# Kernel tuning notes

Hardware: AMD Instinct MI355X
Metric: run time of the kernel (lower is better)

The kernel has to match this reference:

```python
import jax, jax.numpy as jnp
import numpy as np

WH, WW, NUM_HEADS = 7, 7, 16
DIM = 512
B_WINDOWS = 4096   # batch * num_windows
NW = 64            # num_windows per image (mask groups)
N = WH * WW        # 49 tokens per window


def _relative_position_index():
    # Mirrors the torch buffer construction exactly (torch.meshgrid default is 'ij').
    coords = np.stack(np.meshgrid(np.arange(WH), np.arange(WW), indexing='ij'))  # [2,WH,WW]
    cf = coords.reshape(2, -1)                              # [2, N]
    rel = cf[:, :, None] - cf[:, None, :]                   # [2, N, N]
    rel = rel.transpose(1, 2, 0).copy()                     # [N, N, 2]
    rel[:, :, 0] += WH - 1
    rel[:, :, 1] += WW - 1
    rel[:, :, 0] *= 2 * WW - 1
    return jnp.asarray(rel.sum(-1), dtype=jnp.int32)        # [N, N]

REL_IDX = _relative_position_index()


def setup_inputs() -> dict:
    key = jax.random.key(0)
    ks = jax.random.split(key, 7)
    return {
        'x':          jax.random.normal(ks[0], (B_WINDOWS, N, DIM), jnp.float32),
        'mask':       jax.random.normal(ks[1], (NW, N, N), jnp.float32),
        'Wqkv':       jax.random.normal(ks[2], (3 * DIM, DIM), jnp.float32) * (DIM ** -0.5),
        'bqkv':       jax.random.normal(ks[3], (3 * DIM,), jnp.float32) * 0.02,
        'bias_table': jax.random.normal(ks[4], ((2 * WH - 1) * (2 * WW - 1), NUM_HEADS), jnp.float32) * 0.02,
        'Wproj':      jax.random.normal(ks[5], (DIM, DIM), jnp.float32) * (DIM ** -0.5),
        'bproj':      jax.random.normal(ks[6], (DIM,), jnp.float32) * 0.02,
    }


def reference(x, mask, Wqkv, bqkv, bias_table, Wproj, bproj):
    B, n, C = x.shape                      # [B_, 49, 512]
    hd = C // NUM_HEADS
    scale = hd ** -0.5
    qkv = (x @ Wqkv.T + bqkv).reshape(B, n, 3, NUM_HEADS, hd)
    qkv = qkv.transpose(2, 0, 3, 1, 4)     # [3, B, H, N, hd]
    q, k, v = qkv[0] * scale, qkv[1], qkv[2]
    attn = jnp.einsum('bhnd,bhmd->bhnm', q, k)          # [B, H, N, N]
    # gathered relative position bias: [1, H, N, N]
    bias = bias_table[REL_IDX].transpose(2, 0, 1)[None]
    attn = attn + bias
    nW = mask.shape[0]
    attn = attn.reshape(B // nW, nW, NUM_HEADS, n, n) + mask[None, :, None]
    attn = jax.nn.softmax(attn.reshape(B, NUM_HEADS, n, n), axis=-1)
    out = jnp.einsum('bhnm,bhmd->bhnd', attn, v)        # [B, H, N, hd]
    out = out.transpose(0, 2, 1, 3).reshape(B, n, C)
    return out @ Wproj.T + bproj
```

## Files before the change

kernel.cpp:

```cpp
#include <hip/hip_runtime.h>
#include <stdint.h>

#define NHEADS 16
#define DIM 512
#define BWIN 4096
#define NTOK 49
#define M_TOTAL (BWIN * NTOK)
#define QSCALE 0.17677669529663687f

typedef __attribute__((ext_vector_type(4)))  float f32x4;
typedef __attribute__((ext_vector_type(16))) float f32x16;
typedef __attribute__((ext_vector_type(8)))  short s16x8;
typedef __attribute__((ext_vector_type(4)))  short s16x4;

__device__ __forceinline__ f32x4 mfma16(s16x8 a, s16x8 b, f32x4 c) {
    return __builtin_amdgcn_mfma_f32_16x16x32_bf16(a, b, c, 0, 0, 0);
}
__device__ __forceinline__ f32x16 mfma32(s16x8 a, s16x8 b, f32x16 c) {
    return __builtin_amdgcn_mfma_f32_32x32x16_bf16(a, b, c, 0, 0, 0);
}

__device__ __forceinline__ short f2bf(float f) {
    unsigned u = __builtin_bit_cast(unsigned, f);
    u += 0x7FFFu + ((u >> 16) & 1u);
    return (short)(u >> 16);
}

__device__ __forceinline__ unsigned cvtpk(float a, float b) {
    unsigned r;
    asm("v_cvt_pk_bf16_f32 %0, %1, %2" : "=v"(r) : "v"(a), "v"(b));
    return r;
}

__device__ __forceinline__ void gload16(const void* g, void* l) {
    __builtin_amdgcn_global_load_lds(
        (const __attribute__((address_space(1))) void*)g,
        (__attribute__((address_space(3))) void*)l, 16, 0, 0);
}


__global__ void k_prep_x(const float* __restrict__ x, short* __restrict__ xb) {
    int i = blockIdx.x * blockDim.x + threadIdx.x;
    int stride = gridDim.x * blockDim.x;
    const int n4 = M_TOTAL * DIM / 4;
    for (; i < n4; i += stride) {
        f32x4 v = ((const f32x4*)x)[i];
        s16x4 o;
        o[0] = f2bf(v[0]); o[1] = f2bf(v[1]); o[2] = f2bf(v[2]); o[3] = f2bf(v[3]);
        ((s16x4*)xb)[i] = o;
    }
}

__global__ void k_prep_w(const float* __restrict__ src, short* __restrict__ dst,
                         int n, int scale_lim) {
    int i = blockIdx.x * blockDim.x + threadIdx.x;
    int stride = gridDim.x * blockDim.x;
    for (; i < n; i += stride) {
        float v = src[i];
        if (i < scale_lim) v *= QSCALE;
        dst[i] = f2bf(v);
    }
}

__global__ void k_prep_bm(const float* __restrict__ btab, const float* __restrict__ mask,
                          float* __restrict__ bmF) {
    int idx = blockIdx.x * blockDim.x + threadIdx.x;
    int stride = gridDim.x * blockDim.x;
    const int n = 64 * NHEADS * 2 * 2 * 64 * 16;
    for (; idx < n; idx += stride) {
        int r    = idx & 15;
        int lane = (idx >> 4) & 63;
        int it   = (idx >> 10) & 1;
        int jt   = (idx >> 11) & 1;
        int head = (idx >> 12) & 15;
        int w64  = idx >> 16;
        int l31 = lane & 31, h = lane >> 5;
        int i = 32 * it + l31;
        int j = 32 * jt + (r & 3) + 8 * (r >> 2) + 4 * h;
        float v;
        if (j >= 49)      v = -1e30f;
        else if (i >= 49) v = 0.f;
        else {
            int ridx = (i / 7 - j / 7 + 6) * 13 + (i % 7 - j % 7 + 6);
            v = btab[ridx * 16 + head] + mask[(w64 * 49 + i) * 49 + j];
        }
        bmF[idx] = v;
    }
}

template <int MODE>
__global__ __launch_bounds__(512, 2) void k_gemm(
    const short* __restrict__ A, const short* __restrict__ B,
    const float* __restrict__ bias, void* __restrict__ C,
    int ntiles, int nwg) {
    __shared__ short lA[2][256 * 64];
    __shared__ short lB[2][256 * 64];
    const int K = 512;
    const size_t MP = M_TOTAL;

    int bid   = blockIdx.x;
    int chunk = nwg >> 3;
    int wg    = (bid & 7) * chunk + (bid >> 3);
    int mt = wg / ntiles;
    int nt = wg - mt * ntiles;

    int t = threadIdx.x;
    int lane = t & 63, wid = t >> 6;
    int l15 = lane & 15, g = (lane >> 4) & 3;
    int wr = wid >> 2, wc = wid & 3;

    const short* aT = A + (size_t)mt * 256 * K;
    const short* bT = B + (size_t)nt * 256 * K;

    f32x4 acc[8][4] = {};
    s16x8 af[4][2], bf0[2][2], bf1[2][2];

#define STAGE_A(buf, H, kt) do {                                               \
    _Pragma("unroll") for (int j = 0; j < 2; j++) {                            \
        int r_ = j * 128 + (H) * 64 + (t >> 3);                                \
        int sc_ = (t & 7) ^ (r_ & 7);                                          \
        gload16(aT + (size_t)r_ * K + (kt) * 64 + sc_ * 8,                     \
                &lA[buf][r_ * 64 + (t & 7) * 8]);                              \
    } } while (0)

#define STAGE_B(buf, H, kt) do {                                               \
    _Pragma("unroll") for (int j = 0; j < 2; j++) {                            \
        int u_ = j * 64 + (t >> 3);                                            \
        int r_ = ((u_ >> 5) << 6) | ((H) << 5) | (u_ & 31);                    \
        int sc_ = (t & 7) ^ (r_ & 7);                                          \
        gload16(bT + (size_t)r_ * K + (kt) * 64 + sc_ * 8,                     \
                &lB[buf][r_ * 64 + (t & 7) * 8]);                              \
    } } while (0)

#define LDA(MH, cur) do {                                                      \
    const short* pa_ = &lA[cur][(wr * 128 + (MH) * 64 + l15) * 64];            \
    _Pragma("unroll") for (int mi = 0; mi < 4; mi++)                           \
    _Pragma("unroll") for (int ks = 0; ks < 2; ks++)                           \
        af[mi][ks] = *(const s16x8*)(pa_ + mi * 1024 +                         \
                                     (((ks * 4 + g) ^ (l15 & 7)) * 8));        \
    } while (0)

#define LDB(BF, NH, cur) do {                                                  \
    const short* pb_ = &lB[cur][(wc * 64 + (NH) * 32 + l15) * 64];             \
    _Pragma("unroll") for (int nj = 0; nj < 2; nj++)                           \
    _Pragma("unroll") for (int ks = 0; ks < 2; ks++)                           \
        BF[nj][ks] = *(const s16x8*)(pb_ + nj * 1024 +                         \
                                     (((ks * 4 + g) ^ (l15 & 7)) * 8));        \
    } while (0)

#define MMQ(BF, MH, NH) do {                                                   \
    __builtin_amdgcn_s_setprio(1);                                             \
    _Pragma("unroll") for (int ks = 0; ks < 2; ks++)                           \
    _Pragma("unroll") for (int mi = 0; mi < 4; mi++)                           \
    _Pragma("unroll") for (int nj = 0; nj < 2; nj++)                           \
        acc[(MH) * 4 + mi][(NH) * 2 + nj] =                                    \
            mfma16(af[mi][ks], BF[nj][ks], acc[(MH) * 4 + mi][(NH) * 2 + nj]); \
    __builtin_amdgcn_s_setprio(0);                                             \
} while (0)

#define BAR() __builtin_amdgcn_s_barrier()
#define LGW() do { asm volatile("s_waitcnt lgkmcnt(0)" ::: "memory");          \
                   __builtin_amdgcn_sched_barrier(0); } while (0)
#define VMW(st) do {                                                           \
    if (st) asm volatile("s_waitcnt vmcnt(4)" ::: "memory");                   \
    else    asm volatile("s_waitcnt vmcnt(0)" ::: "memory"); } while (0)

    STAGE_A(0, 0, 0);
    STAGE_B(0, 0, 0);
    STAGE_B(0, 1, 0);
    STAGE_A(0, 1, 0);
    asm volatile("s_waitcnt vmcnt(4)" ::: "memory");
    BAR();

    for (int kt = 0; kt < 8; ++kt) {
        const int cur = kt & 1, nxt = cur ^ 1;
        const bool st = kt < 7;
        LDA(0, cur); LDB(bf0, 0, cur);
        if (st) STAGE_A(nxt, 0, kt + 1);
        VMW(st); BAR(); LGW();
        MMQ(bf0, 0, 0);
        BAR();
        LDB(bf1, 1, cur);
        if (st) STAGE_B(nxt, 0, kt + 1);
        VMW(st); BAR(); LGW();
        MMQ(bf1, 0, 1);
        BAR();
        LDA(1, cur);
        if (st) STAGE_B(nxt, 1, kt + 1);
        VMW(st); BAR(); LGW();
        MMQ(bf1, 1, 1);
        BAR();
        if (st) STAGE_A(nxt, 1, kt + 1);
        VMW(st); BAR(); LGW();
        MMQ(bf0, 1, 0);
        BAR();
    }

#undef STAGE_A
#undef STAGE_B
#undef LDA
#undef LDB
#undef MMQ
#undef BAR
#undef LGW
#undef VMW

    int m0 = mt * 256 + wr * 128;
    int n0 = nt * 256 + wc * 64;

    if (MODE == 0) {
        short* region = (wid < 4) ? (&lA[0][0] + wid * 8192)
                                  : (&lB[0][0] + (wid - 4) * 8192);
#pragma unroll
        for (int a = 0; a < 4; a++) {
            int co = (a >> 1) * 32 + (a & 1) * 16;
            int n = n0 + co + l15;
            float bv = bias[n];
            if (n < 512) bv *= QSCALE;
            int w16 = (co >> 3) + (l15 >> 3);
#pragma unroll
            for (int mi = 0; mi < 8; mi++)
#pragma unroll
                for (int r = 0; r < 4; r++) {
                    int row = mi * 16 + g * 4 + r;
                    region[row * 64 + ((w16 ^ (row & 7)) * 8) + (l15 & 7)] =
                        f2bf(acc[mi][a][r] + bv);
                }
        }
#pragma unroll
        for (int p = 0; p < 2; p++) {
            int plane = (n0 >> 5) + p;
            short* dst = (short*)C + ((size_t)plane * MP + m0) * 32;
#pragma unroll
            for (int i = 0; i < 8; i++) {
                int f = i * 64 + lane;
                int row = f >> 2, c = f & 3;
                s16x8 v = *(const s16x8*)(region + row * 64 +
                                          (((p * 4 + c) ^ (row & 7)) * 8));
                *(s16x8*)(dst + (size_t)f * 8) = v;
            }
        }
    } else {
#pragma unroll
        for (int a = 0; a < 4; a++) {
            int co = (a >> 1) * 32 + (a & 1) * 16;
            int n = n0 + co + l15;
            float bv = bias[n];
#pragma unroll
            for (int mi = 0; mi < 8; mi++)
#pragma unroll
                for (int r = 0; r < 4; r++) {
                    int m = m0 + mi * 16 + g * 4 + r;
                    ((float*)C)[(size_t)m * 512 + n] = acc[mi][a][r] + bv;
                }
        }
    }
}

__global__ __launch_bounds__(256, 4) void k_attn(
    const short* __restrict__ qkv, const float* __restrict__ bmF,
    short* __restrict__ ao) {
    int wid = threadIdx.x >> 6, lane = threadIdx.x & 63;
    int p = blockIdx.x * 4 + wid;
    int w = p >> 4, head = p & 15;
    int l31 = lane & 31, h = lane >> 5;
    const size_t MP = M_TOTAL;

    const short* qb = qkv + ((size_t)head * MP + w * 49) * 32;
    const short* kb = qb + (size_t)16 * MP * 32;
    const short* vb = qb + (size_t)32 * MP * 32;

    s16x8 qf[2][2], kf[2][2];
#pragma unroll
    for (int t = 0; t < 2; t++) {
        int row = t * 32 + l31;
#pragma unroll
        for (int s = 0; s < 2; s++) {
            qf[t][s] = *(const s16x8*)(qb + row * 32 + 16 * s + 8 * h);
            kf[t][s] = *(const s16x8*)(kb + row * 32 + 16 * s + 8 * h);
        }
    }

    union U8 { short s[8]; s16x8 v; };
    U8 vf[4];
#pragma unroll
    for (int jc = 0; jc < 4; jc++)
#pragma unroll
        for (int e = 0; e < 8; e++)
            vf[jc].s[e] = vb[(16 * jc + 8 * h + e) * 32 + l31];

    f32x16 st[2][2] = {};
#pragma unroll
    for (int s = 0; s < 2; s++)
#pragma unroll
        for (int jt = 0; jt < 2; jt++)
#pragma unroll
            for (int it = 0; it < 2; it++)
                st[jt][it] = mfma32(kf[jt][s], qf[it][s], st[jt][it]);

    const float* bs = bmF + ((size_t)((w & 63) * NHEADS + head)) * 4096;
#pragma unroll
    for (int jt = 0; jt < 2; jt++)
#pragma unroll
        for (int it = 0; it < 2; it++) {
            const f32x4* bp = (const f32x4*)(bs + (((jt * 2 + it) * 64) + lane) * 16);
            f32x4 b0 = bp[0], b1 = bp[1], b2 = bp[2], b3 = bp[3];
#pragma unroll
            for (int r = 0; r < 4; r++) {
                st[jt][it][r]      += b0[r];
                st[jt][it][4 + r]  += b1[r];
                st[jt][it][8 + r]  += b2[r];
                st[jt][it][12 + r] += b3[r];
            }
        }

    float inv[2];
#pragma unroll
    for (int it = 0; it < 2; it++) {
        float mx = -1e30f;
#pragma unroll
        for (int jt = 0; jt < 2; jt++)
#pragma unroll
            for (int r = 0; r < 16; r++) mx = fmaxf(mx, st[jt][it][r]);
        mx = fmaxf(mx, __shfl_xor(mx, 32));
        float sum = 0.f;
#pragma unroll
        for (int jt = 0; jt < 2; jt++)
#pragma unroll
            for (int r = 0; r < 16; r++) {
                float e = __expf(st[jt][it][r] - mx);
                st[jt][it][r] = e;
                sum += e;
            }
        sum += __shfl_xor(sum, 32);
        inv[it] = 1.0f / sum;
    }

    f32x16 oacc[2] = {};
#pragma unroll
    for (int jc = 0; jc < 4; jc++) {
        const int jt = jc >> 1, rb = 8 * (jc & 1);
#pragma unroll
        for (int it = 0; it < 2; it++) {
            float iv = inv[it];
            unsigned pk0  = cvtpk(st[jt][it][rb + 0] * iv, st[jt][it][rb + 1] * iv);
            unsigned pk0b = cvtpk(st[jt][it][rb + 2] * iv, st[jt][it][rb + 3] * iv);
            unsigned pk1  = cvtpk(st[jt][it][rb + 4] * iv, st[jt][it][rb + 5] * iv);
            unsigned pk1b = cvtpk(st[jt][it][rb + 6] * iv, st[jt][it][rb + 7] * iv);
            unsigned o0  = __shfl_xor(pk0, 32);
            unsigned o0b = __shfl_xor(pk0b, 32);
            unsigned o1  = __shfl_xor(pk1, 32);
            unsigned o1b = __shfl_xor(pk1b, 32);
            union { unsigned d[4]; s16x8 v; } pa;
            pa.d[0] = h ? o1  : pk0;
            pa.d[1] = h ? o1b : pk0b;
            pa.d[2] = h ? pk1 : o0;
            pa.d[3] = h ? pk1b : o0b;
            oacc[it] = mfma32(pa.v, vf[jc].v, oacc[it]);
        }
    }

    short* ob = ao + (size_t)w * 49 * 512 + head * 32 + l31;
#pragma unroll
    for (int it = 0; it < 2; it++)
#pragma unroll
        for (int r = 0; r < 16; r++) {
            int i = 32 * it + 4 * h + (r & 3) + 8 * (r >> 2);
            if (i < 49) ob[(size_t)i * 512] = f2bf(oacc[it][r]);
        }
}


extern "C" void kernel_launch(void* const* d_in, const int* in_sizes, int n_in,
                              void* d_out, int out_size, void* d_ws, size_t ws_size,
                              hipStream_t stream) {
    const float* x     = (const float*)d_in[0];
    const float* mask  = (const float*)d_in[1];
    const float* Wqkv  = (const float*)d_in[2];
    const float* bqkv  = (const float*)d_in[3];
    const float* btab  = (const float*)d_in[4];
    const float* Wproj = (const float*)d_in[5];
    const float* bproj = (const float*)d_in[6];
    float* out = (float*)d_out;

    char* ws = (char*)d_ws;
    size_t off = 0;
    short* xb     = (short*)(ws + off); off += (size_t)M_TOTAL * 512 * 2;
    short* qkvb   = (short*)(ws + off); off += (size_t)48 * M_TOTAL * 32 * 2 + 65536;
    short* Wqkvb  = (short*)(ws + off); off += (size_t)1536 * 512 * 2;
    short* Wprojb = (short*)(ws + off); off += (size_t)512 * 512 * 2;
    float* bmF    = (float*)(ws + off); off += (size_t)64 * NHEADS * 4 * 64 * 16 * 4;
    short* ao = xb;

    k_prep_x<<<2048, 256, 0, stream>>>(x, xb);
    k_prep_w<<<1536, 256, 0, stream>>>(Wqkv, Wqkvb, 1536 * 512, 512 * 512);
    k_prep_w<<<512, 256, 0, stream>>>(Wproj, Wprojb, 512 * 512, 0);
    k_prep_bm<<<4096, 256, 0, stream>>>(btab, mask, bmF);

    k_gemm<0><<<4704, 512, 0, stream>>>(xb, Wqkvb, bqkv, qkvb, 6, 4704);
    k_attn<<<16384, 256, 0, stream>>>(qkvb, bmF, ao);
    k_gemm<1><<<1568, 512, 0, stream>>>(ao, Wprojb, bproj, out, 2, 1568);
}
```

Baseline: 1.049 ms.

## Fuse fp32-to-bf16 conversion of x into the QKV GEMM A-tile load path

Removes the separate k_prep_x kernel. The QKV GEMM now reads x in fp32 into registers, converts it to bf16 with v_cvt_pk_bf16_f32 and writes it into swizzled LDS, with the global loads rescheduled around the existing double-buffered pipeline. This avoids one full read of x and one write and read of a bf16 copy. In exchange, every N-tile block re-reads and re-converts its A rows in fp32, which doubles A-side bytes unless L2 catches the reuse. A-tile loads now pass through VGPRs instead of going straight to LDS, which raises register pressure under the 2-blocks-per-CU launch bound.

```diff
diff --git a/kernel.cpp b/kernel.cpp
--- a/kernel.cpp
+++ b/kernel.cpp
@@ -38,18 +38,6 @@
         (__attribute__((address_space(3))) void*)l, 16, 0, 0);
 }
 
-
-__global__ void k_prep_x(const float* __restrict__ x, short* __restrict__ xb) {
-    int i = blockIdx.x * blockDim.x + threadIdx.x;
-    int stride = gridDim.x * blockDim.x;
-    const int n4 = M_TOTAL * DIM / 4;
-    for (; i < n4; i += stride) {
-        f32x4 v = ((const f32x4*)x)[i];
-        s16x4 o;
-        o[0] = f2bf(v[0]); o[1] = f2bf(v[1]); o[2] = f2bf(v[2]); o[3] = f2bf(v[3]);
-        ((s16x4*)xb)[i] = o;
-    }
-}
 
 __global__ void k_prep_w(const float* __restrict__ src, short* __restrict__ dst,
                          int n, int scale_lim) {
@@ -90,7 +78,8 @@
 
 template <int MODE>
 __global__ __launch_bounds__(512, 2) void k_gemm(
-    const short* __restrict__ A, const short* __restrict__ B,
+    const float* __restrict__ Af, const short* __restrict__ Ab,
+    const short* __restrict__ B,
     const float* __restrict__ bias, void* __restrict__ C,
     int ntiles, int nwg) {
     __shared__ short lA[2][256 * 64];
@@ -109,17 +98,19 @@
     int l15 = lane & 15, g = (lane >> 4) & 3;
     int wr = wid >> 2, wc = wid & 3;
 
-    const short* aT = A + (size_t)mt * 256 * K;
-    const short* bT = B + (size_t)nt * 256 * K;
+    const float* aTf = Af + (size_t)mt * 256 * K;
+    const short* aTb = Ab + (size_t)mt * 256 * K;
+    const short* bT  = B  + (size_t)nt * 256 * K;
 
     f32x4 acc[8][4] = {};
     s16x8 af[4][2], bf0[2][2], bf1[2][2];
+    f32x4 rh0[2][2], rh1[2][2];
 
 #define STAGE_A(buf, H, kt) do {                                               \
     _Pragma("unroll") for (int j = 0; j < 2; j++) {                            \
         int r_ = j * 128 + (H) * 64 + (t >> 3);                                \
         int sc_ = (t & 7) ^ (r_ & 7);                                          \
-        gload16(aT + (size_t)r_ * K + (kt) * 64 + sc_ * 8,                     \
+        gload16(aTb + (size_t)r_ * K + (kt) * 64 + sc_ * 8,                    \
                 &lA[buf][r_ * 64 + (t & 7) * 8]);                              \
     } } while (0)
 
@@ -130,6 +121,24 @@
         int sc_ = (t & 7) ^ (r_ & 7);                                          \
         gload16(bT + (size_t)r_ * K + (kt) * 64 + sc_ * 8,                     \
                 &lB[buf][r_ * 64 + (t & 7) * 8]);                              \
+    } } while (0)
+
+#define LOADA_F(R, H, kt) do {                                                 \
+    _Pragma("unroll") for (int j = 0; j < 2; j++) {                            \
+        int r_ = j * 128 + (H) * 64 + (t >> 3);                                \
+        const float* p_ = aTf + (size_t)r_ * K + (kt) * 64 + (t & 7) * 8;      \
+        R[j][0] = *(const f32x4*)p_; R[j][1] = *(const f32x4*)(p_ + 4);        \
+    } } while (0)
+
+#define WRA_F(buf, H, R) do {                                                  \
+    _Pragma("unroll") for (int j = 0; j < 2; j++) {                            \
+        int r_ = j * 128 + (H) * 64 + (t >> 3);                                \
+        union { unsigned d[4]; s16x8 v; } u_;                                  \
+        u_.d[0] = cvtpk(R[j][0][0], R[j][0][1]);                               \
+        u_.d[1] = cvtpk(R[j][0][2], R[j][0][3]);                               \
+        u_.d[2] = cvtpk(R[j][1][0], R[j][1][1]);                               \
+        u_.d[3] = cvtpk(R[j][1][2], R[j][1][3]);                               \
+        *(s16x8*)(&lA[buf][r_ * 64 + (((t & 7) ^ (r_ & 7)) * 8)]) = u_.v;      \
     } } while (0)
 
 #define LDA(MH, cur) do {                                                      \
@@ -161,54 +170,95 @@
 #define BAR() __builtin_amdgcn_s_barrier()
 #define LGW() do { asm volatile("s_waitcnt lgkmcnt(0)" ::: "memory");          \
                    __builtin_amdgcn_sched_barrier(0); } while (0)
-#define VMW(st) do {                                                           \
-    if (st) asm volatile("s_waitcnt vmcnt(4)" ::: "memory");                   \
-    else    asm volatile("s_waitcnt vmcnt(0)" ::: "memory"); } while (0)
-
-    STAGE_A(0, 0, 0);
-    STAGE_B(0, 0, 0);
-    STAGE_B(0, 1, 0);
-    STAGE_A(0, 1, 0);
-    asm volatile("s_waitcnt vmcnt(4)" ::: "memory");
-    BAR();
-
-    for (int kt = 0; kt < 8; ++kt) {
-        const int cur = kt & 1, nxt = cur ^ 1;
-        const bool st = kt < 7;
-        LDA(0, cur); LDB(bf0, 0, cur);
-        if (st) STAGE_A(nxt, 0, kt + 1);
-        VMW(st); BAR(); LGW();
-        MMQ(bf0, 0, 0);
+#define VMWN(n) asm volatile("s_waitcnt vmcnt(" #n ")" ::: "memory")
+
+    if constexpr (MODE == 0) {
+        LOADA_F(rh0, 0, 0);
+        LOADA_F(rh1, 1, 0);
+        STAGE_B(0, 0, 0);
+        STAGE_B(0, 1, 0);
+        VMWN(8);  WRA_F(0, 0, rh0);
+        VMWN(4);  WRA_F(0, 1, rh1);
+        VMWN(2);
+        LGW();
         BAR();
-        LDB(bf1, 1, cur);
-        if (st) STAGE_B(nxt, 0, kt + 1);
-        VMW(st); BAR(); LGW();
-        MMQ(bf1, 0, 1);
+
+        for (int kt = 0; kt < 8; ++kt) {
+            const int cur = kt & 1, nxt = cur ^ 1;
+            const bool st = kt < 7;
+            LDA(0, cur); LDB(bf0, 0, cur);
+            if (st) { LOADA_F(rh0, 0, kt + 1); VMWN(4); }
+            else    VMWN(0);
+            BAR(); LGW();
+            MMQ(bf0, 0, 0);
+            BAR();
+            LDB(bf1, 1, cur);
+            if (st) { LOADA_F(rh1, 1, kt + 1); STAGE_B(nxt, 0, kt + 1); VMWN(6); }
+            BAR(); LGW();
+            MMQ(bf1, 0, 1);
+            BAR();
+            LDA(1, cur);
+            if (st) { STAGE_B(nxt, 1, kt + 1); VMWN(4); WRA_F(nxt, 0, rh0); }
+            BAR(); LGW();
+            MMQ(bf1, 1, 1);
+            BAR();
+            if (st) { WRA_F(nxt, 1, rh1); VMWN(2); }
+            BAR(); LGW();
+            MMQ(bf0, 1, 0);
+            BAR();
+        }
+    } else {
+        STAGE_A(0, 0, 0);
+        STAGE_B(0, 0, 0);
+        STAGE_B(0, 1, 0);
+        STAGE_A(0, 1, 0);
+        VMWN(4);
         BAR();
-        LDA(1, cur);
-        if (st) STAGE_B(nxt, 1, kt + 1);
-        VMW(st); BAR(); LGW();
-        MMQ(bf1, 1, 1);
-        BAR();
-        if (st) STAGE_A(nxt, 1, kt + 1);
-        VMW(st); BAR(); LGW();
-        MMQ(bf0, 1, 0);
-        BAR();
+
+        for (int kt = 0; kt < 8; ++kt) {
+            const int cur = kt & 1, nxt = cur ^ 1;
+            const bool st = kt < 7;
+            LDA(0, cur); LDB(bf0, 0, cur);
+            if (st) STAGE_A(nxt, 0, kt + 1);
+            if (st) VMWN(4); else VMWN(0);
+            BAR(); LGW();
+            MMQ(bf0, 0, 0);
+            BAR();
+            LDB(bf1, 1, cur);
+            if (st) STAGE_B(nxt, 0, kt + 1);
+            if (st) VMWN(4); else VMWN(0);
+            BAR(); LGW();
+            MMQ(bf1, 0, 1);
+            BAR();
+            LDA(1, cur);
+            if (st) STAGE_B(nxt, 1, kt + 1);
+            if (st) VMWN(4); else VMWN(0);
+            BAR(); LGW();
+            MMQ(bf1, 1, 1);
+            BAR();
+            if (st) STAGE_A(nxt, 1, kt + 1);
+            if (st) VMWN(4); else VMWN(0);
+            BAR(); LGW();
+            MMQ(bf0, 1, 0);
+            BAR();
+        }
     }
 
 #undef STAGE_A
 #undef STAGE_B
+#undef LOADA_F
+#undef WRA_F
 #undef LDA
 #undef LDB
 #undef MMQ
 #undef BAR
 #undef LGW
-#undef VMW
+#undef VMWN
 
     int m0 = mt * 256 + wr * 128;
     int n0 = nt * 256 + wc * 64;
 
-    if (MODE == 0) {
+    if constexpr (MODE == 0) {
         short* region = (wid < 4) ? (&lA[0][0] + wid * 8192)
                                   : (&lB[0][0] + (wid - 4) * 8192);
 #pragma unroll
@@ -385,19 +435,17 @@
 
     char* ws = (char*)d_ws;
     size_t off = 0;
-    short* xb     = (short*)(ws + off); off += (size_t)M_TOTAL * 512 * 2;
+    short* ao     = (short*)(ws + off); off += (size_t)M_TOTAL * 512 * 2;
     short* qkvb   = (short*)(ws + off); off += (size_t)48 * M_TOTAL * 32 * 2 + 65536;
     short* Wqkvb  = (short*)(ws + off); off += (size_t)1536 * 512 * 2;
     short* Wprojb = (short*)(ws + off); off += (size_t)512 * 512 * 2;
     float* bmF    = (float*)(ws + off); off += (size_t)64 * NHEADS * 4 * 64 * 16 * 4;
-    short* ao = xb;
-
-    k_prep_x<<<2048, 256, 0, stream>>>(x, xb);
+
     k_prep_w<<<1536, 256, 0, stream>>>(Wqkv, Wqkvb, 1536 * 512, 512 * 512);
     k_prep_w<<<512, 256, 0, stream>>>(Wproj, Wprojb, 512 * 512, 0);
     k_prep_bm<<<4096, 256, 0, stream>>>(btab, mask, bmF);
 
-    k_gemm<0><<<4704, 512, 0, stream>>>(xb, Wqkvb, bqkv, qkvb, 6, 4704);
+    k_gemm<0><<<4704, 512, 0, stream>>>(x, nullptr, Wqkvb, bqkv, qkvb, 6, 4704);
     k_attn<<<16384, 256, 0, stream>>>(qkvb, bmF, ao);
-    k_gemm<1><<<1568, 512, 0, stream>>>(ao, Wprojb, bproj, out, 2, 1568);
-}
+    k_gemm<1><<<1568, 512, 0, stream>>>(nullptr, ao, Wprojb, bproj, out, 2, 1568);
+}
```

Measured after the change: 1.089 ms. +3.8%, slower.

## Halve GEMM K-tile to 32 to fit four blocks per CU

Applied to the files above, without the earlier changes.

The GEMM's LDS K-tile shrinks from 64 to 32, which halves shared memory per block. Launch bounds rise to 4 blocks of 512 threads per CU, and the loop runs 16 K-steps instead of 8 with matching load, wait and swizzle changes. The epilogue for the QKV layout now stages output in two 64-row passes so it fits the smaller LDS buffers. More resident blocks should hide latency better, but the register cap falls, which risks spilling the 128-float accumulator, and the extra barriers per step add overhead.

```diff
diff --git a/kernel.cpp b/kernel.cpp
--- a/kernel.cpp
+++ b/kernel.cpp
@@ -89,12 +89,12 @@
 }
 
 template <int MODE>
-__global__ __launch_bounds__(512, 2) void k_gemm(
+__global__ __launch_bounds__(512, 4) void k_gemm(
     const short* __restrict__ A, const short* __restrict__ B,
     const float* __restrict__ bias, void* __restrict__ C,
     int ntiles, int nwg) {
-    __shared__ short lA[2][256 * 64];
-    __shared__ short lB[2][256 * 64];
+    __shared__ short lA[2][256 * 32];
+    __shared__ short lB[2][256 * 32];
     const int K = 512;
     const size_t MP = M_TOTAL;
 
@@ -113,48 +113,41 @@
     const short* bT = B + (size_t)nt * 256 * K;
 
     f32x4 acc[8][4] = {};
-    s16x8 af[4][2], bf0[2][2], bf1[2][2];
+    s16x8 af[4], bf0[2], bf1[2];
 
 #define STAGE_A(buf, H, kt) do {                                               \
-    _Pragma("unroll") for (int j = 0; j < 2; j++) {                            \
-        int r_ = j * 128 + (H) * 64 + (t >> 3);                                \
-        int sc_ = (t & 7) ^ (r_ & 7);                                          \
-        gload16(aT + (size_t)r_ * K + (kt) * 64 + sc_ * 8,                     \
-                &lA[buf][r_ * 64 + (t & 7) * 8]);                              \
-    } } while (0)
+    int r_ = ((t >> 8) << 7) + (H) * 64 + ((t >> 2) & 63);                     \
+    int sc_ = (t & 3) ^ (r_ & 3);                                              \
+    gload16(aT + (size_t)r_ * K + (kt) * 32 + sc_ * 8,                         \
+            &lA[buf][r_ * 32 + (t & 3) * 8]);                                  \
+} while (0)
 
 #define STAGE_B(buf, H, kt) do {                                               \
-    _Pragma("unroll") for (int j = 0; j < 2; j++) {                            \
-        int u_ = j * 64 + (t >> 3);                                            \
-        int r_ = ((u_ >> 5) << 6) | ((H) << 5) | (u_ & 31);                    \
-        int sc_ = (t & 7) ^ (r_ & 7);                                          \
-        gload16(bT + (size_t)r_ * K + (kt) * 64 + sc_ * 8,                     \
-                &lB[buf][r_ * 64 + (t & 7) * 8]);                              \
-    } } while (0)
+    int u_ = t >> 2;                                                           \
+    int r_ = ((u_ >> 5) << 6) | ((H) << 5) | (u_ & 31);                        \
+    int sc_ = (t & 3) ^ (r_ & 3);                                              \
+    gload16(bT + (size_t)r_ * K + (kt) * 32 + sc_ * 8,                         \
+            &lB[buf][r_ * 32 + (t & 3) * 8]);                                  \
+} while (0)
 
 #define LDA(MH, cur) do {                                                      \
-    const short* pa_ = &lA[cur][(wr * 128 + (MH) * 64 + l15) * 64];            \
+    const short* pa_ = &lA[cur][(wr * 128 + (MH) * 64 + l15) * 32];            \
     _Pragma("unroll") for (int mi = 0; mi < 4; mi++)                           \
-    _Pragma("unroll") for (int ks = 0; ks < 2; ks++)                           \
-        af[mi][ks] = *(const s16x8*)(pa_ + mi * 1024 +                         \
-                                     (((ks * 4 + g) ^ (l15 & 7)) * 8));        \
-    } while (0)
+        af[mi] = *(const s16x8*)(pa_ + mi * 512 + (((g) ^ (l15 & 3)) * 8));    \
+} while (0)
 
 #define LDB(BF, NH, cur) do {                                                  \
-    const short* pb_ = &lB[cur][(wc * 64 + (NH) * 32 + l15) * 64];             \
+    const short* pb_ = &lB[cur][(wc * 64 + (NH) * 32 + l15) * 32];             \
     _Pragma("unroll") for (int nj = 0; nj < 2; nj++)                           \
-    _Pragma("unroll") for (int ks = 0; ks < 2; ks++)                           \
-        BF[nj][ks] = *(const s16x8*)(pb_ + nj * 1024 +                         \
-                                     (((ks * 4 + g) ^ (l15 & 7)) * 8));        \
-    } while (0)
+        BF[nj] = *(const s16x8*)(pb_ + nj * 512 + (((g) ^ (l15 & 3)) * 8));    \
+} while (0)
 
 #define MMQ(BF, MH, NH) do {                                                   \
     __builtin_amdgcn_s_setprio(1);                                             \
-    _Pragma("unroll") for (int ks = 0; ks < 2; ks++)                           \
     _Pragma("unroll") for (int mi = 0; mi < 4; mi++)                           \
     _Pragma("unroll") for (int nj = 0; nj < 2; nj++)                           \
         acc[(MH) * 4 + mi][(NH) * 2 + nj] =                                    \
-            mfma16(af[mi][ks], BF[nj][ks], acc[(MH) * 4 + mi][(NH) * 2 + nj]); \
+            mfma16(af[mi], BF[nj], acc[(MH) * 4 + mi][(NH) * 2 + nj]);         \
     __builtin_amdgcn_s_setprio(0);                                             \
 } while (0)
 
@@ -162,19 +155,19 @@
 #define LGW() do { asm volatile("s_waitcnt lgkmcnt(0)" ::: "memory");          \
                    __builtin_amdgcn_sched_barrier(0); } while (0)
 #define VMW(st) do {                                                           \
-    if (st) asm volatile("s_waitcnt vmcnt(4)" ::: "memory");                   \
+    if (st) asm volatile("s_waitcnt vmcnt(2)" ::: "memory");                   \
     else    asm volatile("s_waitcnt vmcnt(0)" ::: "memory"); } while (0)
 
     STAGE_A(0, 0, 0);
     STAGE_B(0, 0, 0);
     STAGE_B(0, 1, 0);
     STAGE_A(0, 1, 0);
-    asm volatile("s_waitcnt vmcnt(4)" ::: "memory");
+    asm volatile("s_waitcnt vmcnt(2)" ::: "memory");
     BAR();
 
-    for (int kt = 0; kt < 8; ++kt) {
+    for (int kt = 0; kt < 16; ++kt) {
         const int cur = kt & 1, nxt = cur ^ 1;
-        const bool st = kt < 7;
+        const bool st = kt < 15;
         LDA(0, cur); LDB(bf0, 0, cur);
         if (st) STAGE_A(nxt, 0, kt + 1);
         VMW(st); BAR(); LGW();
@@ -209,35 +202,39 @@
     int n0 = nt * 256 + wc * 64;
 
     if (MODE == 0) {
-        short* region = (wid < 4) ? (&lA[0][0] + wid * 8192)
-                                  : (&lB[0][0] + (wid - 4) * 8192);
-#pragma unroll
-        for (int a = 0; a < 4; a++) {
-            int co = (a >> 1) * 32 + (a & 1) * 16;
-            int n = n0 + co + l15;
-            float bv = bias[n];
-            if (n < 512) bv *= QSCALE;
-            int w16 = (co >> 3) + (l15 >> 3);
-#pragma unroll
-            for (int mi = 0; mi < 8; mi++)
-#pragma unroll
-                for (int r = 0; r < 4; r++) {
-                    int row = mi * 16 + g * 4 + r;
-                    region[row * 64 + ((w16 ^ (row & 7)) * 8) + (l15 & 7)] =
-                        f2bf(acc[mi][a][r] + bv);
+        short* region = (wid < 4) ? (&lA[0][0] + wid * 4096)
+                                  : (&lB[0][0] + (wid - 4) * 4096);
+#pragma unroll
+        for (int pass = 0; pass < 2; ++pass) {
+#pragma unroll
+            for (int a = 0; a < 4; a++) {
+                int co = (a >> 1) * 32 + (a & 1) * 16;
+                int n = n0 + co + l15;
+                float bv = bias[n];
+                if (n < 512) bv *= QSCALE;
+                int w16 = (co >> 3) + (l15 >> 3);
+#pragma unroll
+                for (int mi2 = 0; mi2 < 4; mi2++) {
+#pragma unroll
+                    for (int r = 0; r < 4; r++) {
+                        int row = mi2 * 16 + g * 4 + r;
+                        region[row * 64 + ((w16 ^ (row & 7)) * 8) + (l15 & 7)] =
+                            f2bf(acc[pass * 4 + mi2][a][r] + bv);
+                    }
                 }
-        }
-#pragma unroll
-        for (int p = 0; p < 2; p++) {
-            int plane = (n0 >> 5) + p;
-            short* dst = (short*)C + ((size_t)plane * MP + m0) * 32;
-#pragma unroll
-            for (int i = 0; i < 8; i++) {
-                int f = i * 64 + lane;
-                int row = f >> 2, c = f & 3;
-                s16x8 v = *(const s16x8*)(region + row * 64 +
-                                          (((p * 4 + c) ^ (row & 7)) * 8));
-                *(s16x8*)(dst + (size_t)f * 8) = v;
+            }
+#pragma unroll
+            for (int p2 = 0; p2 < 2; p2++) {
+                int plane = (n0 >> 5) + p2;
+                short* dst = (short*)C + ((size_t)plane * MP + m0 + pass * 64) * 32;
+#pragma unroll
+                for (int i = 0; i < 4; i++) {
+                    int f = i * 64 + lane;
+                    int row = f >> 2, c = f & 3;
+                    s16x8 v = *(const s16x8*)(region + row * 64 +
+                                              (((p2 * 4 + c) ^ (row & 7)) * 8));
+                    *(s16x8*)(dst + (size_t)f * 8) = v;
+                }
             }
         }
     } else {
```

After: 4.038 ms. 285% more time.
